# Kernel optimization log

Hardware: AMD Instinct MI355X
Metric: run time of the kernel (lower is better)

Reference implementation:

```python
import jax, jax.numpy as jnp
import numpy as np

B = 64       # graphs per batch
n = 512      # nodes per graph (equal-size graphs)
F_IN = 128
F_HID = 128
F_OUT = 64
DEGREES = (2, 2)
AVG_DEG = 16


def setup_inputs() -> dict:
    key = jax.random.key(0)
    ks = jax.random.split(key, 12)
    N = B * n
    X = jax.random.normal(ks[0], (N, F_IN), dtype=jnp.float32)
    batch = jnp.repeat(jnp.arange(B, dtype=jnp.int64), n)
    # within-graph edges: a ring (guarantees no isolated nodes, so the
    # per-graph trimming in the original keeps all n nodes) + random edges
    E_rand = N * (AVG_DEG - 1)
    g = jax.random.randint(ks[1], (E_rand,), 0, B, dtype=jnp.int64)
    src_l = jax.random.randint(ks[2], (E_rand,), 0, n, dtype=jnp.int64)
    dst_l = jax.random.randint(ks[3], (E_rand,), 0, n, dtype=jnp.int64)
    src_r = jnp.arange(N, dtype=jnp.int64)
    dst_r = (src_r // n) * n + (src_r % n + 1) % n
    src = jnp.concatenate([g * n + src_l, src_r])
    dst = jnp.concatenate([g * n + dst_l, dst_r])
    edge_index = jnp.stack([src, dst])  # [2, 524288]
    xav = lambda k, sh: jax.random.normal(k, sh, dtype=jnp.float32) * np.sqrt(2.0 / (sh[-2] + sh[-1])).astype(np.float32)
    W1 = xav(ks[4], (DEGREES[0] + 1, F_IN, F_HID))
    b1 = jnp.zeros((F_HID,), jnp.float32)
    W2 = xav(ks[5], (DEGREES[1] + 1, F_HID, F_HID))
    b2 = jnp.zeros((F_HID,), jnp.float32)
    Wout = xav(ks[6], (F_HID, F_OUT))
    bout = jnp.zeros((F_OUT,), jnp.float32)
    alpha = jnp.float32(0.5)
    return {"X": X, "batch": batch, "edge_index": edge_index,
            "W1": W1, "b1": b1, "W2": W2, "b2": b2,
            "Wout": Wout, "bout": bout, "alpha": alpha}


def _conv(Xb, S, Ws, b):
    # out = sum_k S^k @ X @ W_k + b, then ReLU. Xb: [B,n,F], S: [B,n,n]
    out = jnp.einsum('bnf,fg->bng', Xb, Ws[0])
    Sx = Xb
    for k in range(1, Ws.shape[0]):
        Sx = jnp.einsum('bnm,bmf->bnf', S, Sx)
        out = out + jnp.einsum('bnf,fg->bng', Sx, Ws[k])
    return jax.nn.relu(out + b)


def reference(X, batch, edge_index, W1, b1, W2, b2, Wout, bout, alpha):
    src, dst = edge_index[0], edge_index[1]
    g = src // n  # edges are within-graph, so graph id from src
    # dense per-graph adjacency (== block-diag S of the original,
    # batched instead of one big [N,N] block-diagonal matrix)
    adj = jnp.zeros((B, n, n), jnp.float32).at[g, src % n, dst % n].add(1.0)
    S = alpha * adj + (1.0 - alpha) * jnp.eye(n, dtype=jnp.float32)
    x = X.reshape(B, n, -1)
    x = _conv(x, S, W1, b1)
    x = _conv(x, S, W2, b2)
    pooled = jnp.max(x, axis=1)          # global_max_pool -> [B, F_HID]
    return pooled @ Wout + bout          # [B, F_OUT]
```

## Files before the change

kernel.cpp:

```cpp
#include <hip/hip_runtime.h>
#include <hip/hip_bf16.h>

#define F 128
#define NG 512

typedef __attribute__((ext_vector_type(8))) short s16x8;
typedef __attribute__((ext_vector_type(4))) float f32x4;

__device__ inline float bf2f(unsigned short u) {
    unsigned int x = ((unsigned int)u) << 16;
    return __builtin_bit_cast(float, x);
}
__device__ inline unsigned short f2bf(float f) {
    __hip_bfloat16 h = __float2bfloat16(f);
    return __builtin_bit_cast(unsigned short, h);
}
__device__ inline unsigned int pack16(float x, float y) {
    return (unsigned int)f2bf(x) | ((unsigned int)f2bf(y) << 16);
}

typedef const __attribute__((address_space(1))) unsigned int guint;
typedef __attribute__((address_space(3))) unsigned int luint;
__device__ inline void stage16(const void* g, void* l) {
    __builtin_amdgcn_global_load_lds((guint*)g, (luint*)l, 16, 0, 0);
}

__device__ inline s16x8 sfrag4(unsigned w, int kbase, int row, float alpha, float diagv) {
    s16x8 a;
    #pragma unroll
    for (int j = 0; j < 8; ++j) {
        float v = alpha * (float)((w >> (4 * j)) & 0xFu);
        if (kbase + j == row) v += diagv;
        a[j] = (short)f2bf(v);
    }
    return a;
}


__global__ __launch_bounds__(256) void prep_kernel(const float* __restrict__ X,
                                                   unsigned short* __restrict__ Xr,
                                                   unsigned short* __restrict__ Xc,
                                                   const float* __restrict__ W1,
                                                   const float* __restrict__ W2,
                                                   unsigned short* __restrict__ o1,
                                                   unsigned short* __restrict__ o2,
                                                   uint4* __restrict__ cntz) {
    __shared__ unsigned short tile[64][F + 4];
    int tid = threadIdx.x;
    if (blockIdx.x < 512) {
        int g = blockIdx.x >> 3;
        int nt = blockIdx.x & 7;
        int node0 = nt * 64;
        const float* Xg = X + ((size_t)g * NG + node0) * F;
        unsigned short* Xrg = Xr + ((size_t)g * NG + node0) * F;
        #pragma unroll
        for (int u = tid; u < 64 * 32; u += 256) {
            int row = u >> 5, c4 = u & 31;
            float4 v = ((const float4*)(Xg + (size_t)row * F))[c4];
            unsigned short a0 = f2bf(v.x), a1 = f2bf(v.y), a2 = f2bf(v.z), a3 = f2bf(v.w);
            tile[row][c4 * 4 + 0] = a0;
            tile[row][c4 * 4 + 1] = a1;
            tile[row][c4 * 4 + 2] = a2;
            tile[row][c4 * 4 + 3] = a3;
            uint2 w;
            w.x = (unsigned int)a0 | ((unsigned int)a1 << 16);
            w.y = (unsigned int)a2 | ((unsigned int)a3 << 16);
            ((uint2*)(Xrg + (size_t)row * F))[c4] = w;
        }
        __syncthreads();
        unsigned short* Xcg = Xc + (size_t)g * F * NG;
        #pragma unroll
        for (int u = tid; u < F * 16; u += 256) {
            int f = u >> 4, nb = u & 15;
            int n0 = nb * 4;
            uint2 w;
            w.x = (unsigned int)tile[n0 + 0][f] | ((unsigned int)tile[n0 + 1][f] << 16);
            w.y = (unsigned int)tile[n0 + 2][f] | ((unsigned int)tile[n0 + 3][f] << 16);
            ((uint2*)(Xcg + (size_t)f * NG + node0))[nb] = w;
        }
    } else if (blockIdx.x < 896) {
        int t = (blockIdx.x - 512) * 256 + tid;
        const float* W = (t < 49152) ? W1 : W2;
        unsigned short* o = (t < 49152) ? o1 : o2;
        int tt = (t < 49152) ? t : t - 49152;
        int j = tt & 7;
        int lane = (tt >> 3) & 63;
        int ct = (tt >> 9) & 7;
        int ks = tt >> 12;
        int k = ks * 32 + (lane >> 4) * 8 + j;
        int c = ct * 16 + (lane & 15);
        o[tt] = f2bf(W[(size_t)k * F + c]);
    } else {
        size_t base = (size_t)(blockIdx.x - 896) * 1024;
        uint4 z = {0u, 0u, 0u, 0u};
        #pragma unroll
        for (int i = 0; i < 4; ++i) cntz[base + i * 256 + tid] = z;
    }
}


__global__ void cnt_scatter_kernel(const int* __restrict__ src, const int* __restrict__ dst,
                                   unsigned int* __restrict__ cnt4, int E) {
    int e = blockIdx.x * blockDim.x + threadIdx.x;
    if (e >= E) return;
    int s = src[e], d = dst[e];
    size_t idx = ((size_t)s << 9) | (unsigned)(d & (NG - 1));
    atomicAdd(&cnt4[idx >> 3], 1u << ((idx & 7) * 4));
}


__global__ __launch_bounds__(512) void sapply_kernel(
    const unsigned int* __restrict__ cnt4, const float* __restrict__ alphap,
    const unsigned short* __restrict__ Bc, unsigned short* __restrict__ Cc) {
    __shared__ unsigned short Bs[65536];
    const int p = blockIdx.x;
    const int id = ((p & 7) << 5) | (p >> 3);
    const int g = id >> 2, rt = id & 3;
    const int tid = threadIdx.x, wave = tid >> 6, lane = tid & 63;
    const int l15 = lane & 15, hi = lane >> 4;
    const int lrow = wave * 16 + l15;
    const int row = rt * 128 + lrow;
    const float alpha = *alphap;
    const float diagv = 1.0f - alpha;

    const unsigned short* Bcg = Bc + (size_t)g * F * NG;
    #pragma unroll
    for (int it = 0; it < 16; ++it) {
        int f = it * 8 + wave;
        stage16(Bcg + (size_t)f * NG + ((lane ^ (f & 7)) << 3), Bs + f * 512);
    }
    __syncthreads();

    f32x4 acc[8];
    #pragma unroll
    for (int ct = 0; ct < 8; ++ct) acc[ct] = (f32x4){0.f, 0.f, 0.f, 0.f};

    const unsigned int* crow = cnt4 + ((size_t)g * NG + row) * 64;
    const int bxor = l15 & 7;
    #pragma unroll 4
    for (int ks = 0; ks < 16; ++ks) {
        s16x8 a = sfrag4(crow[ks * 4 + hi], ks * 32 + hi * 8, row, alpha, diagv);
        #pragma unroll
        for (int ct = 0; ct < 8; ++ct) {
            int col = ct * 16 + l15;
            s16x8 b = *(const s16x8*)(Bs + col * 512 + ((((ks << 2) | hi) ^ bxor) << 3));
            acc[ct] = __builtin_amdgcn_mfma_f32_16x16x32_bf16(a, b, acc[ct], 0, 0, 0);
        }
    }

    const int rloc = wave * 16 + (hi << 2);
    unsigned short* Ccg = Cc + (size_t)g * F * NG + rt * 128 + rloc;
    #pragma unroll
    for (int ct = 0; ct < 8; ++ct) {
        int col = ct * 16 + l15;
        uint2 w;
        w.x = pack16(acc[ct][0], acc[ct][1]);
        w.y = pack16(acc[ct][2], acc[ct][3]);
        *(uint2*)(Ccg + (size_t)col * NG) = w;
    }
}


template <int WRITE_H>
__global__ __launch_bounds__(512) void fused_conv_kernel(
    const unsigned int* __restrict__ cnt4, const float* __restrict__ alphap,
    const unsigned short* __restrict__ Bc, const unsigned short* __restrict__ A0,
    const unsigned short* __restrict__ Wswz, const float* __restrict__ bias,
    unsigned short* __restrict__ Hr, unsigned short* __restrict__ Hc,
    float* __restrict__ pooledp) {
    __shared__ unsigned short Bs[65536];
    const int p = blockIdx.x;
    const int id = ((p & 7) << 5) | (p >> 3);
    const int g = id >> 2, rt = id & 3;
    const int tid = threadIdx.x, wave = tid >> 6, lane = tid & 63;
    const int l15 = lane & 15, hi = lane >> 4;
    const int lrow = wave * 16 + l15;
    const int row = rt * 128 + lrow;
    const float alpha = *alphap;
    const float diagv = 1.0f - alpha;

    const unsigned short* Bcg = Bc + (size_t)g * F * NG;
    #pragma unroll
    for (int it = 0; it < 16; ++it) {
        int f = it * 8 + wave;
        stage16(Bcg + (size_t)f * NG + ((lane ^ (f & 7)) << 3), Bs + f * 512);
    }
    __syncthreads();

    f32x4 sacc[8];
    #pragma unroll
    for (int ct = 0; ct < 8; ++ct) sacc[ct] = (f32x4){0.f, 0.f, 0.f, 0.f};
    {
        const unsigned int* crow = cnt4 + ((size_t)g * NG + row) * 64;
        const int bxor = l15 & 7;
        #pragma unroll 4
        for (int ks = 0; ks < 16; ++ks) {
            s16x8 a = sfrag4(crow[ks * 4 + hi], ks * 32 + hi * 8, row, alpha, diagv);
            #pragma unroll
            for (int ct = 0; ct < 8; ++ct) {
                int col = ct * 16 + l15;
                s16x8 b = *(const s16x8*)(Bs + col * 512 + ((((ks << 2) | hi) ^ bxor) << 3));
                sacc[ct] = __builtin_amdgcn_mfma_f32_16x16x32_bf16(a, b, sacc[ct], 0, 0, 0);
            }
        }
    }

    s16x8 a1f[4];
    #pragma unroll
    for (int kk = 0; kk < 4; ++kk) {
        int f0 = kk * 32 + hi * 8;
        s16x8 t;
        #pragma unroll
        for (int j = 0; j < 8; ++j)
            t[j] = (short)Bs[(f0 + j) * 512 + (((row >> 3) ^ j) << 3) + (row & 7)];
        a1f[kk] = t;
    }
    __syncthreads();

    {
        int rloc = wave * 16 + (hi << 2);
        #pragma unroll
        for (int ct = 0; ct < 8; ++ct) {
            int col = ct * 16 + l15;
            #pragma unroll
            for (int r = 0; r < 4; ++r)
                Bs[(rloc + r) * 136 + col] = f2bf(sacc[ct][r]);
        }
    }
    __syncthreads();

    f32x4 acc[8];
    #pragma unroll
    for (int ct = 0; ct < 8; ++ct) acc[ct] = (f32x4){0.f, 0.f, 0.f, 0.f};
    const int arow = id * 128 + lrow;
    #pragma unroll
    for (int ks = 0; ks < 12; ++ks) {
        s16x8 a;
        if (ks < 4) {
            a = *(const s16x8*)(A0 + (size_t)arow * F + ks * 32 + hi * 8);
        } else if (ks < 8) {
            a = a1f[ks - 4];
        } else {
            a = *(const s16x8*)(Bs + lrow * 136 + (ks - 8) * 32 + hi * 8);
        }
        const unsigned short* wb = Wswz + ((size_t)ks * 512 + lane) * 8;
        #pragma unroll
        for (int ct = 0; ct < 8; ++ct) {
            s16x8 b = *(const s16x8*)(wb + (size_t)ct * 512);
            acc[ct] = __builtin_amdgcn_mfma_f32_16x16x32_bf16(a, b, acc[ct], 0, 0, 0);
        }
    }

    const int rloc = wave * 16 + (hi << 2);
    if (WRITE_H) {
        unsigned short* OutS = Bs + 40960;
        #pragma unroll
        for (int ct = 0; ct < 8; ++ct) {
            int col = ct * 16 + l15;
            float b = bias[col];
            float v0 = fmaxf(acc[ct][0] + b, 0.f);
            float v1 = fmaxf(acc[ct][1] + b, 0.f);
            float v2 = fmaxf(acc[ct][2] + b, 0.f);
            float v3 = fmaxf(acc[ct][3] + b, 0.f);
            uint2 w;
            w.x = pack16(v0, v1);
            w.y = pack16(v2, v3);
            *(uint2*)(Hc + (size_t)g * F * NG + (size_t)col * NG + rt * 128 + rloc) = w;
            OutS[(rloc + 0) * F + col] = f2bf(v0);
            OutS[(rloc + 1) * F + col] = f2bf(v1);
            OutS[(rloc + 2) * F + col] = f2bf(v2);
            OutS[(rloc + 3) * F + col] = f2bf(v3);
        }
        __syncthreads();
        uint4* o4 = (uint4*)(Hr + ((size_t)g * NG + rt * 128) * F);
        const uint4* s4 = (const uint4*)OutS;
        #pragma unroll
        for (int u = tid; u < 128 * F / 8; u += 512) o4[u] = s4[u];
    } else {
        __syncthreads();
        float* wmax = (float*)Bs;
        #pragma unroll
        for (int ct = 0; ct < 8; ++ct) {
            int col = ct * 16 + l15;
            float b = bias[col];
            float m = fmaxf(fmaxf(acc[ct][0], acc[ct][1]), fmaxf(acc[ct][2], acc[ct][3]));
            m = fmaxf(m + b, 0.f);
            m = fmaxf(m, __shfl_xor(m, 16));
            m = fmaxf(m, __shfl_xor(m, 32));
            if (lane < 16) wmax[wave * F + col] = m;
        }
        __syncthreads();
        if (tid < F) {
            float m = wmax[tid];
            #pragma unroll
            for (int w = 1; w < 8; ++w) m = fmaxf(m, wmax[w * F + tid]);
            pooledp[((size_t)rt * 64 + g) * F + tid] = m;
        }
    }
}


__global__ __launch_bounds__(64) void out_gemm_kernel(const float* __restrict__ pooledp,
                                                      const float* __restrict__ Wout,
                                                      const float* __restrict__ bout,
                                                      float* __restrict__ out) {
    __shared__ float p[F];
    int b = blockIdx.x, t = threadIdx.x;
    #pragma unroll
    for (int c = t; c < F; c += 64) {
        float m = pooledp[(size_t)b * F + c];
        m = fmaxf(m, pooledp[((size_t)64 + b) * F + c]);
        m = fmaxf(m, pooledp[((size_t)128 + b) * F + c]);
        m = fmaxf(m, pooledp[((size_t)192 + b) * F + c]);
        p[c] = m;
    }
    __syncthreads();
    float acc = bout[t];
    #pragma unroll 8
    for (int k = 0; k < F; ++k) acc += p[k] * Wout[k * 64 + t];
    out[(size_t)b * 64 + t] = acc;
}


extern "C" void kernel_launch(void* const* d_in, const int* in_sizes, int n_in,
                              void* d_out, int out_size, void* d_ws, size_t ws_size,
                              hipStream_t stream) {
    const float* X     = (const float*)d_in[0];
    const int*   ei    = (const int*)d_in[2];
    const float* W1    = (const float*)d_in[3];
    const float* b1    = (const float*)d_in[4];
    const float* W2    = (const float*)d_in[5];
    const float* b2    = (const float*)d_in[6];
    const float* Wout  = (const float*)d_in[7];
    const float* bout  = (const float*)d_in[8];
    const float* alpha = (const float*)d_in[9];

    const int N = in_sizes[0] / F;
    const int E = in_sizes[2] / 2;
    const int Bg = N / NG;

    const int* srcv = ei;
    const int* dstv = ei + E;

    char* ws = (char*)d_ws;
    const size_t CBYTES = (size_t)Bg * NG * NG / 2;
    const size_t PBYTES = (size_t)N * F * 2;

    unsigned int* cnt4 = (unsigned int*)ws;
    unsigned short* P0 = (unsigned short*)(ws + CBYTES);
    unsigned short* P1 = (unsigned short*)(ws + CBYTES + PBYTES);
    unsigned short* P3 = (unsigned short*)(ws + CBYTES + 2 * PBYTES);
    char* tail = ws + CBYTES + 3 * PBYTES;
    unsigned short* Wswz1 = (unsigned short*)tail;
    unsigned short* Wswz2 = Wswz1 + (size_t)3 * F * F;
    float* pooledp = (float*)(Wswz2 + (size_t)3 * F * F);

    prep_kernel<<<1408, 256, 0, stream>>>(X, P0, P1, W1, W2, Wswz1, Wswz2, (uint4*)cnt4);

    cnt_scatter_kernel<<<(E + 255) / 256, 256, 0, stream>>>(srcv, dstv, cnt4, E);

    sapply_kernel<<<Bg * 4, 512, 0, stream>>>(cnt4, alpha, P1, P3);
    fused_conv_kernel<1><<<Bg * 4, 512, 0, stream>>>(cnt4, alpha, P3, P0, Wswz1, b1, P0, P1, nullptr);

    sapply_kernel<<<Bg * 4, 512, 0, stream>>>(cnt4, alpha, P1, P3);
    fused_conv_kernel<0><<<Bg * 4, 512, 0, stream>>>(cnt4, alpha, P3, P0, Wswz2, b2, nullptr, nullptr, pooledp);

    out_gemm_kernel<<<Bg, 64, 0, stream>>>(pooledp, Wout, bout, (float*)d_out);
}
```

Before: 110.6 us.

## Drop row-major activation copies and fuse output GEMM into last conv block

Removes the row-major bf16 copies of X and the hidden layer, so the fused conv kernel reads the column-major buffer instead. It stages that slice into a new LDS tile and gathers transposed fragments from it. The final pooling reduction and output GEMM now run in the last-finishing block of the second conv kernel, selected by an atomic done counter, which removes a separate launch. This trades extra LDS use and strided LDS gathers for fewer global writes and one fewer kernel.

```diff
diff --git a/kernel.cpp b/kernel.cpp
--- a/kernel.cpp
+++ b/kernel.cpp
@@ -38,13 +38,13 @@
 
 
 __global__ __launch_bounds__(256) void prep_kernel(const float* __restrict__ X,
-                                                   unsigned short* __restrict__ Xr,
                                                    unsigned short* __restrict__ Xc,
                                                    const float* __restrict__ W1,
                                                    const float* __restrict__ W2,
                                                    unsigned short* __restrict__ o1,
                                                    unsigned short* __restrict__ o2,
-                                                   uint4* __restrict__ cntz) {
+                                                   uint4* __restrict__ cntz,
+                                                   unsigned int* __restrict__ donectr) {
     __shared__ unsigned short tile[64][F + 4];
     int tid = threadIdx.x;
     if (blockIdx.x < 512) {
@@ -52,20 +52,14 @@
         int nt = blockIdx.x & 7;
         int node0 = nt * 64;
         const float* Xg = X + ((size_t)g * NG + node0) * F;
-        unsigned short* Xrg = Xr + ((size_t)g * NG + node0) * F;
         #pragma unroll
         for (int u = tid; u < 64 * 32; u += 256) {
             int row = u >> 5, c4 = u & 31;
             float4 v = ((const float4*)(Xg + (size_t)row * F))[c4];
-            unsigned short a0 = f2bf(v.x), a1 = f2bf(v.y), a2 = f2bf(v.z), a3 = f2bf(v.w);
-            tile[row][c4 * 4 + 0] = a0;
-            tile[row][c4 * 4 + 1] = a1;
-            tile[row][c4 * 4 + 2] = a2;
-            tile[row][c4 * 4 + 3] = a3;
-            uint2 w;
-            w.x = (unsigned int)a0 | ((unsigned int)a1 << 16);
-            w.y = (unsigned int)a2 | ((unsigned int)a3 << 16);
-            ((uint2*)(Xrg + (size_t)row * F))[c4] = w;
+            tile[row][c4 * 4 + 0] = f2bf(v.x);
+            tile[row][c4 * 4 + 1] = f2bf(v.y);
+            tile[row][c4 * 4 + 2] = f2bf(v.z);
+            tile[row][c4 * 4 + 3] = f2bf(v.w);
         }
         __syncthreads();
         unsigned short* Xcg = Xc + (size_t)g * F * NG;
@@ -91,6 +85,7 @@
         int c = ct * 16 + (lane & 15);
         o[tt] = f2bf(W[(size_t)k * F + c]);
     } else {
+        if (blockIdx.x == 896 && tid == 0) *donectr = 0;
         size_t base = (size_t)(blockIdx.x - 896) * 1024;
         uint4 z = {0u, 0u, 0u, 0u};
         #pragma unroll
@@ -164,11 +159,13 @@
 template <int WRITE_H>
 __global__ __launch_bounds__(512) void fused_conv_kernel(
     const unsigned int* __restrict__ cnt4, const float* __restrict__ alphap,
-    const unsigned short* __restrict__ Bc, const unsigned short* __restrict__ A0,
+    const unsigned short* __restrict__ Bc, const unsigned short* __restrict__ A0c,
     const unsigned short* __restrict__ Wswz, const float* __restrict__ bias,
-    unsigned short* __restrict__ Hr, unsigned short* __restrict__ Hc,
-    float* __restrict__ pooledp) {
+    unsigned short* __restrict__ Hc, float* __restrict__ pooledp,
+    unsigned int* __restrict__ donectr, const float* __restrict__ Wout,
+    const float* __restrict__ bout, float* __restrict__ outp) {
     __shared__ unsigned short Bs[65536];
+    __shared__ unsigned short Ts[16384];
     const int p = blockIdx.x;
     const int id = ((p & 7) << 5) | (p >> 3);
     const int g = id >> 2, rt = id & 3;
@@ -185,6 +182,12 @@
         int f = it * 8 + wave;
         stage16(Bcg + (size_t)f * NG + ((lane ^ (f & 7)) << 3), Bs + f * 512);
     }
+    const unsigned short* A0g = A0c + (size_t)g * F * NG + rt * 128;
+    #pragma unroll
+    for (int j = 0; j < 4; ++j) {
+        int fb = (j * 8 + wave) * 4;
+        stage16(A0g + (size_t)(fb + (lane >> 4)) * NG + ((lane & 15) << 3), Ts + fb * 128);
+    }
     __syncthreads();
 
     f32x4 sacc[8];
@@ -232,12 +235,15 @@
     f32x4 acc[8];
     #pragma unroll
     for (int ct = 0; ct < 8; ++ct) acc[ct] = (f32x4){0.f, 0.f, 0.f, 0.f};
-    const int arow = id * 128 + lrow;
     #pragma unroll
     for (int ks = 0; ks < 12; ++ks) {
         s16x8 a;
         if (ks < 4) {
-            a = *(const s16x8*)(A0 + (size_t)arow * F + ks * 32 + hi * 8);
+            s16x8 t;
+            #pragma unroll
+            for (int j = 0; j < 8; ++j)
+                t[j] = (short)Ts[(ks * 32 + hi * 8 + j) * 128 + lrow];
+            a = t;
         } else if (ks < 8) {
             a = a1f[ks - 4];
         } else {
@@ -253,7 +259,6 @@
 
     const int rloc = wave * 16 + (hi << 2);
     if (WRITE_H) {
-        unsigned short* OutS = Bs + 40960;
         #pragma unroll
         for (int ct = 0; ct < 8; ++ct) {
             int col = ct * 16 + l15;
@@ -266,16 +271,7 @@
             w.x = pack16(v0, v1);
             w.y = pack16(v2, v3);
             *(uint2*)(Hc + (size_t)g * F * NG + (size_t)col * NG + rt * 128 + rloc) = w;
-            OutS[(rloc + 0) * F + col] = f2bf(v0);
-            OutS[(rloc + 1) * F + col] = f2bf(v1);
-            OutS[(rloc + 2) * F + col] = f2bf(v2);
-            OutS[(rloc + 3) * F + col] = f2bf(v3);
-        }
-        __syncthreads();
-        uint4* o4 = (uint4*)(Hr + ((size_t)g * NG + rt * 128) * F);
-        const uint4* s4 = (const uint4*)OutS;
-        #pragma unroll
-        for (int u = tid; u < 128 * F / 8; u += 512) o4[u] = s4[u];
+        }
     } else {
         __syncthreads();
         float* wmax = (float*)Bs;
@@ -296,29 +292,35 @@
             for (int w = 1; w < 8; ++w) m = fmaxf(m, wmax[w * F + tid]);
             pooledp[((size_t)rt * 64 + g) * F + tid] = m;
         }
-    }
-}
-
-
-__global__ __launch_bounds__(64) void out_gemm_kernel(const float* __restrict__ pooledp,
-                                                      const float* __restrict__ Wout,
-                                                      const float* __restrict__ bout,
-                                                      float* __restrict__ out) {
-    __shared__ float p[F];
-    int b = blockIdx.x, t = threadIdx.x;
-    #pragma unroll
-    for (int c = t; c < F; c += 64) {
-        float m = pooledp[(size_t)b * F + c];
-        m = fmaxf(m, pooledp[((size_t)64 + b) * F + c]);
-        m = fmaxf(m, pooledp[((size_t)128 + b) * F + c]);
-        m = fmaxf(m, pooledp[((size_t)192 + b) * F + c]);
-        p[c] = m;
-    }
-    __syncthreads();
-    float acc = bout[t];
-    #pragma unroll 8
-    for (int k = 0; k < F; ++k) acc += p[k] * Wout[k * 64 + t];
-    out[(size_t)b * 64 + t] = acc;
+        __threadfence();
+        __syncthreads();
+        unsigned int* flagp = (unsigned int*)Bs;
+        if (tid == 0) {
+            unsigned int old = __hip_atomic_fetch_add(donectr, 1u, __ATOMIC_ACQ_REL,
+                                                      __HIP_MEMORY_SCOPE_AGENT);
+            flagp[0] = (old == (unsigned)(gridDim.x - 1)) ? 1u : 0u;
+        }
+        __syncthreads();
+        if (flagp[0]) {
+            __threadfence();
+            int b = tid >> 3;
+            int og = (tid & 7) * 8;
+            float acch[8];
+            #pragma unroll
+            for (int o = 0; o < 8; ++o) acch[o] = bout[og + o];
+            for (int k = 0; k < F; ++k) {
+                float pm = pooledp[(size_t)b * F + k];
+                pm = fmaxf(pm, pooledp[(size_t)(64 + b) * F + k]);
+                pm = fmaxf(pm, pooledp[(size_t)(128 + b) * F + k]);
+                pm = fmaxf(pm, pooledp[(size_t)(192 + b) * F + k]);
+                const float* wr = Wout + (size_t)k * 64 + og;
+                #pragma unroll
+                for (int o = 0; o < 8; ++o) acch[o] += pm * wr[o];
+            }
+            #pragma unroll
+            for (int o = 0; o < 8; ++o) outp[(size_t)b * 64 + og + o] = acch[o];
+        }
+    }
 }
 
 
@@ -347,23 +349,23 @@
     const size_t PBYTES = (size_t)N * F * 2;
 
     unsigned int* cnt4 = (unsigned int*)ws;
-    unsigned short* P0 = (unsigned short*)(ws + CBYTES);
-    unsigned short* P1 = (unsigned short*)(ws + CBYTES + PBYTES);
-    unsigned short* P3 = (unsigned short*)(ws + CBYTES + 2 * PBYTES);
-    char* tail = ws + CBYTES + 3 * PBYTES;
+    unsigned short* P1 = (unsigned short*)(ws + CBYTES);
+    unsigned short* P3 = (unsigned short*)(ws + CBYTES + PBYTES);
+    char* tail = ws + CBYTES + 2 * PBYTES;
     unsigned short* Wswz1 = (unsigned short*)tail;
     unsigned short* Wswz2 = Wswz1 + (size_t)3 * F * F;
     float* pooledp = (float*)(Wswz2 + (size_t)3 * F * F);
-
-    prep_kernel<<<1408, 256, 0, stream>>>(X, P0, P1, W1, W2, Wswz1, Wswz2, (uint4*)cnt4);
+    unsigned int* donectr = (unsigned int*)(pooledp + 4 * 64 * F);
+
+    prep_kernel<<<1408, 256, 0, stream>>>(X, P1, W1, W2, Wswz1, Wswz2, (uint4*)cnt4, donectr);
 
     cnt_scatter_kernel<<<(E + 255) / 256, 256, 0, stream>>>(srcv, dstv, cnt4, E);
 
     sapply_kernel<<<Bg * 4, 512, 0, stream>>>(cnt4, alpha, P1, P3);
-    fused_conv_kernel<1><<<Bg * 4, 512, 0, stream>>>(cnt4, alpha, P3, P0, Wswz1, b1, P0, P1, nullptr);
+    fused_conv_kernel<1><<<Bg * 4, 512, 0, stream>>>(cnt4, alpha, P3, P1, Wswz1, b1, P1,
+                                                     nullptr, nullptr, nullptr, nullptr, nullptr);
 
     sapply_kernel<<<Bg * 4, 512, 0, stream>>>(cnt4, alpha, P1, P3);
-    fused_conv_kernel<0><<<Bg * 4, 512, 0, stream>>>(cnt4, alpha, P3, P0, Wswz2, b2, nullptr, nullptr, pooledp);
-
-    out_gemm_kernel<<<Bg, 64, 0, stream>>>(pooledp, Wout, bout, (float*)d_out);
-}
+    fused_conv_kernel<0><<<Bg * 4, 512, 0, stream>>>(cnt4, alpha, P3, P1, Wswz2, b2, nullptr,
+                                                     pooledp, donectr, Wout, bout, (float*)d_out);
+}
```

New measurement: 154.3 us. +39.5%, slower.
